# Kernel tuning notes

Measured on AMD Instinct MI355X. Metric: run time of the kernel, lower is better.

The kernel has to match this reference:

```python
import jax, jax.numpy as jnp
import numpy as np

B, C, H, W, N = 16, 8, 512, 512, 16384


def setup_inputs() -> dict:
    key = jax.random.key(0)
    k0, k1, k2 = jax.random.split(key, 3)
    prediction = jax.random.normal(k0, (B, C, H, W), dtype=jnp.float32)
    intervals_comp_0 = jax.random.randint(k1, (B, C, N, 2, 2), 0, H, dtype=jnp.int64)
    intervals_comp_1 = jax.random.randint(k2, (B, C, N, 2, 2), 0, H, dtype=jnp.int64)
    return {
        "prediction": prediction,
        "intervals_comp_0": intervals_comp_0,
        "intervals_comp_1": intervals_comp_1,
    }


def _interval_diff(prediction, intervals):
    # prediction: (B, C, H, W); intervals: (B, C, N, 2, 2)
    b, c, n = intervals.shape[:3]
    flat = intervals.reshape(b * c * n, 2, 2)
    # sample/class indices per flattened interval (row-major over (b, c, n))
    s_idx = jnp.repeat(jnp.arange(b), c * n)
    c_idx = jnp.tile(jnp.repeat(jnp.arange(c), n), b)
    birth = prediction[s_idx, c_idx, flat[:, 0, 0], flat[:, 0, 1]]
    death = prediction[s_idx, c_idx, flat[:, 1, 0], flat[:, 1, 1]]
    return jnp.sum((birth - death) ** 2) / b


def reference(prediction, intervals_comp_0, intervals_comp_1):
    loss_0 = _interval_diff(prediction, intervals_comp_0)
    loss_1 = _interval_diff(prediction, intervals_comp_1)
    return loss_0 + loss_1
```

## Files before the change

kernel.cpp:

```cpp
#include <hip/hip_runtime.h>

constexpr int kN      = 16384;
constexpr int kNTOT   = 16 * 8 * 16384;

__device__ __forceinline__ double wave_reduce_sum(double x) {
#pragma unroll
    for (int o = 32; o > 0; o >>= 1) x += __shfl_down(x, o, 64);
    return x;
}

__global__ __launch_bounds__(256) void bd_partial_kernel(
        const float* __restrict__ pred,
        const int*   __restrict__ iv0,
        const int*   __restrict__ iv1,
        double*      __restrict__ partials) {
    const int tid    = blockIdx.x * blockDim.x + threadIdx.x;
    const int stride = gridDim.x * blockDim.x;

    double acc = 0.0;
    for (int i = tid; i < kNTOT; i += stride) {
        const int bc = i >> 14;
        const float* plane = pred + ((size_t)bc << 18);

        const int4 a = *reinterpret_cast<const int4*>(iv0 + 4ll * i);
        const float d0 = plane[(a.x << 9) + a.y] - plane[(a.z << 9) + a.w];

        const int4 b = *reinterpret_cast<const int4*>(iv1 + 4ll * i);
        const float d1 = plane[(b.x << 9) + b.y] - plane[(b.z << 9) + b.w];

        acc += (double)d0 * (double)d0 + (double)d1 * (double)d1;
    }

    acc = wave_reduce_sum(acc);
    __shared__ double s[4];
    const int lane = threadIdx.x & 63;
    const int wid  = threadIdx.x >> 6;
    if (lane == 0) s[wid] = acc;
    __syncthreads();
    if (threadIdx.x == 0) {
        partials[blockIdx.x] = s[0] + s[1] + s[2] + s[3];
    }
}

__global__ __launch_bounds__(256) void bd_final_kernel(
        const double* __restrict__ partials, int n, float* __restrict__ out) {
    double acc = 0.0;
    for (int i = threadIdx.x; i < n; i += 256) acc += partials[i];
    acc = wave_reduce_sum(acc);
    __shared__ double s[4];
    const int lane = threadIdx.x & 63;
    const int wid  = threadIdx.x >> 6;
    if (lane == 0) s[wid] = acc;
    __syncthreads();
    if (threadIdx.x == 0) {
        out[0] = (float)((s[0] + s[1] + s[2] + s[3]) * (1.0 / 16.0));
    }
}

extern "C" void kernel_launch(void* const* d_in, const int* in_sizes, int n_in,
                              void* d_out, int out_size, void* d_ws, size_t ws_size,
                              hipStream_t stream) {
    const float* pred = (const float*)d_in[0];
    const int*   iv0  = (const int*)d_in[1];
    const int*   iv1  = (const int*)d_in[2];
    float*  out      = (float*)d_out;
    double* partials = (double*)d_ws;

    constexpr int kBlocks = 2048;
    bd_partial_kernel<<<kBlocks, 256, 0, stream>>>(pred, iv0, iv1, partials);
    bd_final_kernel<<<1, 256, 0, stream>>>(partials, kBlocks, out);
}
```

Measured before the change: 278.5 us.

## Partition planes across XCDs and split interval sets per wave with prefetch

```diff
diff --git a/kernel.cpp b/kernel.cpp
--- a/kernel.cpp
+++ b/kernel.cpp
@@ -1,7 +1,16 @@
 #include <hip/hip_runtime.h>
 
-constexpr int kN      = 16384;
-constexpr int kNTOT   = 16 * 8 * 16384;
+
+typedef int int4v __attribute__((ext_vector_type(4)));
+
+constexpr int kXcds         = 8;
+constexpr int kPlanesPerXcd = 16;
+constexpr int kItemsPerXcd  = kPlanesPerXcd << 14;
+constexpr int kBlocksPerXcd = 256;
+constexpr int kBlocks       = kBlocksPerXcd * kXcds;
+constexpr int kWavesPerXcd  = kBlocksPerXcd * 4;
+constexpr int kItemsPerStep = (kWavesPerXcd / 2) * 64;
+constexpr int kSteps        = kItemsPerXcd / kItemsPerStep;
 
 __device__ __forceinline__ double wave_reduce_sum(double x) {
 #pragma unroll
@@ -14,32 +23,40 @@
         const int*   __restrict__ iv0,
         const int*   __restrict__ iv1,
         double*      __restrict__ partials) {
-    const int tid    = blockIdx.x * blockDim.x + threadIdx.x;
-    const int stride = gridDim.x * blockDim.x;
+    const int xcd  = blockIdx.x & 7;
+    const int wv   = (blockIdx.x >> 3) * 4 + (threadIdx.x >> 6);
+    const int lane = threadIdx.x & 63;
+    const int set  = wv & 1;
+    const int slot = (wv >> 1) * 64 + lane;
+
+    const int4v* q = reinterpret_cast<const int4v*>(set ? iv1 : iv0);
+
+    int i = xcd * kItemsPerXcd + slot;
+    int4v a = __builtin_nontemporal_load(q + i);
 
     double acc = 0.0;
-    for (int i = tid; i < kNTOT; i += stride) {
-        const int bc = i >> 14;
-        const float* plane = pred + ((size_t)bc << 18);
+#pragma unroll
+    for (int s = 0; s < kSteps; ++s) {
+        const float* plane = pred + ((size_t)(i >> 14) << 18);
 
-        const int4 a = *reinterpret_cast<const int4*>(iv0 + 4ll * i);
-        const float d0 = plane[(a.x << 9) + a.y] - plane[(a.z << 9) + a.w];
+        const float birth = plane[(a.x << 9) + a.y];
+        const float death = plane[(a.z << 9) + a.w];
 
-        const int4 b = *reinterpret_cast<const int4*>(iv1 + 4ll * i);
-        const float d1 = plane[(b.x << 9) + b.y] - plane[(b.z << 9) + b.w];
+        if (s + 1 < kSteps) {
+            i += kItemsPerStep;
+            a = __builtin_nontemporal_load(q + i);
+        }
 
-        acc += (double)d0 * (double)d0 + (double)d1 * (double)d1;
+        const float d = birth - death;
+        acc += (double)d * (double)d;
     }
 
     acc = wave_reduce_sum(acc);
-    __shared__ double s[4];
-    const int lane = threadIdx.x & 63;
-    const int wid  = threadIdx.x >> 6;
-    if (lane == 0) s[wid] = acc;
+    __shared__ double sm[4];
+    const int wid = threadIdx.x >> 6;
+    if (lane == 0) sm[wid] = acc;
     __syncthreads();
-    if (threadIdx.x == 0) {
-        partials[blockIdx.x] = s[0] + s[1] + s[2] + s[3];
-    }
+    if (threadIdx.x == 0) partials[blockIdx.x] = sm[0] + sm[1] + sm[2] + sm[3];
 }
 
 __global__ __launch_bounds__(256) void bd_final_kernel(
@@ -47,14 +64,13 @@
     double acc = 0.0;
     for (int i = threadIdx.x; i < n; i += 256) acc += partials[i];
     acc = wave_reduce_sum(acc);
-    __shared__ double s[4];
+    __shared__ double sm[4];
     const int lane = threadIdx.x & 63;
     const int wid  = threadIdx.x >> 6;
-    if (lane == 0) s[wid] = acc;
+    if (lane == 0) sm[wid] = acc;
     __syncthreads();
-    if (threadIdx.x == 0) {
-        out[0] = (float)((s[0] + s[1] + s[2] + s[3]) * (1.0 / 16.0));
-    }
+    if (threadIdx.x == 0)
+        out[0] = (float)((sm[0] + sm[1] + sm[2] + sm[3]) * (1.0 / 16.0));
 }
 
 extern "C" void kernel_launch(void* const* d_in, const int* in_sizes, int n_in,
@@ -66,7 +82,6 @@
     float*  out      = (float*)d_out;
     double* partials = (double*)d_ws;
 
-    constexpr int kBlocks = 2048;
     bd_partial_kernel<<<kBlocks, 256, 0, stream>>>(pred, iv0, iv1, partials);
     bd_final_kernel<<<1, 256, 0, stream>>>(partials, kBlocks, out);
 }
```

After: 271.5 us. -2.5%, faster.
